# Kernel optimization log

Hardware: AMD Instinct MI355X
Metric: run time of the kernel (lower is better)

The kernel has to match this reference:

```python
import jax, jax.numpy as jnp
import numpy as np

D = 1024
T = 32768


def setup_inputs() -> dict:
    key = jax.random.key(0)
    k1, k2, k3 = jax.random.split(key, 3)
    r_star = jax.random.normal(k1, (D,), dtype=jnp.float32)
    q_t = jax.random.normal(k2, (T, D), dtype=jnp.float32)
    W = jax.random.normal(k3, (D,), dtype=jnp.float32) * (2.0 / D) ** 0.5  # ~GlorotNormal
    b = jnp.zeros((1,), dtype=jnp.float32)
    return {"r_star": r_star, "q_t": q_t, "W": W, "b": b}


def reference(r_star, q_t, W, b):
    # beta_stars[t] = W * (r_star * q_t[t]) + b  -> [T, D]
    beta = W[None, :] * (r_star[None, :] * q_t) + b  # fused elementwise
    # tf.nn.softmax default axis=-1 (over D)
    alpha = jax.nn.softmax(beta, axis=-1)  # [T, D]
    # weighted sum over the T axis -> [D]
    q_t_star = jnp.sum(alpha * q_t, axis=0)
    return q_t_star
```

## Files before the change

kernel.cpp:

```cpp
#include <hip/hip_runtime.h>
#include <math.h>

constexpr int D_   = 1024;
constexpr int T_   = 32768;
constexpr int TPB  = 512;
constexpr int WPB  = TPB / 64;
constexpr int NBLK = 512;
constexpr int TOTW = NBLK * WPB;
constexpr int ROWS = T_ / TOTW;
constexpr int NC4  = D_ / 4;

typedef float f32x4 __attribute__((ext_vector_type(4)));

__global__ __launch_bounds__(TPB) void attn_pass1_fixed(
    const float* __restrict__ r_star,
    const float* __restrict__ q_t,
    const float* __restrict__ W,
    float* __restrict__ partialT)
{
    __shared__ f32x4 lds4[WPB * NC4];

    const int tid  = threadIdx.x;
    const int lane = tid & 63;
    const int wv   = tid >> 6;
    const int gw   = blockIdx.x * WPB + wv;

    constexpr float LOG2E = 1.4426950408889634f;

    const f32x4* r4 = reinterpret_cast<const f32x4*>(r_star);
    const f32x4* w4 = reinterpret_cast<const f32x4*>(W);
    f32x4 s[4];
#pragma unroll
    for (int k = 0; k < 4; ++k)
        s[k] = r4[lane + 64 * k] * w4[lane + 64 * k] * LOG2E;

    f32x4 acc[4];
#pragma unroll
    for (int k = 0; k < 4; ++k) acc[k] = (f32x4)(0.f);

    const f32x4* qb = reinterpret_cast<const f32x4*>(q_t);
    size_t off = (size_t)gw * NC4 + lane;
    constexpr size_t STR = (size_t)TOTW * NC4;

    f32x4 q[4];
#pragma unroll
    for (int k = 0; k < 4; ++k) q[k] = qb[off + 64 * k];

#pragma unroll
    for (int i = 0; i < ROWS; ++i) {
        f32x4 qn[4];
        if (i + 1 < ROWS) {
            off += STR;
#pragma unroll
            for (int k = 0; k < 4; ++k) qn[k] = qb[off + 64 * k];
        }

        f32x4 bb[4];
#pragma unroll
        for (int k = 0; k < 4; ++k) {
            const f32x4 t = s[k] * q[k];
            bb[k].x = exp2f(t.x);
            bb[k].y = exp2f(t.y);
            bb[k].z = exp2f(t.z);
            bb[k].w = exp2f(t.w);
        }
        const float s0 = ((bb[0].x + bb[0].y) + (bb[0].z + bb[0].w))
                       + ((bb[1].x + bb[1].y) + (bb[1].z + bb[1].w));
        const float s1 = ((bb[2].x + bb[2].y) + (bb[2].z + bb[2].w))
                       + ((bb[3].x + bb[3].y) + (bb[3].z + bb[3].w));
        float ssum = s0 + s1;
#pragma unroll
        for (int o = 32; o > 0; o >>= 1)
            ssum += __shfl_xor(ssum, o, 64);

        const float inv = __builtin_amdgcn_rcpf(ssum);
#pragma unroll
        for (int k = 0; k < 4; ++k) {
            const f32x4 a = bb[k] * inv;
            acc[k].x = fmaf(a.x, q[k].x, acc[k].x);
            acc[k].y = fmaf(a.y, q[k].y, acc[k].y);
            acc[k].z = fmaf(a.z, q[k].z, acc[k].z);
            acc[k].w = fmaf(a.w, q[k].w, acc[k].w);
        }
        if (i + 1 < ROWS) {
#pragma unroll
            for (int k = 0; k < 4; ++k) q[k] = qn[k];
        }
    }

#pragma unroll
    for (int k = 0; k < 4; ++k) lds4[wv * NC4 + lane + 64 * k] = acc[k];
    __syncthreads();
    if (tid < NC4) {
        f32x4 sum = lds4[tid];
        for (int w = 1; w < WPB; ++w) sum += lds4[w * NC4 + tid];
        reinterpret_cast<f32x4*>(partialT)[(size_t)tid * NBLK + blockIdx.x] = sum;
    }
}

__global__ __launch_bounds__(TPB) void attn_pass2t(
    const float* __restrict__ partialT,
    float* __restrict__ out)
{
    __shared__ f32x4 red[TPB];
    const int tid = threadIdx.x;
    const int c   = blockIdx.x;
    red[tid] = reinterpret_cast<const f32x4*>(partialT)[(size_t)c * NBLK + tid];
    __syncthreads();
#pragma unroll
    for (int s = TPB / 2; s >= 1; s >>= 1) {
        if (tid < s) red[tid] += red[tid + s];
        __syncthreads();
    }
    if (tid == 0)
        reinterpret_cast<f32x4*>(out)[c] = red[0];
}

__global__ __launch_bounds__(TPB) void attn_pass1_generic(
    const float* __restrict__ r_star,
    const float* __restrict__ q_t,
    const float* __restrict__ W,
    float* __restrict__ partial)
{
    __shared__ f32x4 lds4[WPB * NC4];
    const int tid  = threadIdx.x;
    const int lane = tid & 63;
    const int wv   = tid >> 6;
    const int totalWaves = gridDim.x * WPB;
    const int gw = blockIdx.x * WPB + wv;
    constexpr float LOG2E = 1.4426950408889634f;

    const f32x4* r4 = reinterpret_cast<const f32x4*>(r_star);
    const f32x4* w4 = reinterpret_cast<const f32x4*>(W);
    f32x4 s[4];
#pragma unroll
    for (int k = 0; k < 4; ++k)
        s[k] = r4[lane + 64 * k] * w4[lane + 64 * k] * LOG2E;
    f32x4 acc[4];
#pragma unroll
    for (int k = 0; k < 4; ++k) acc[k] = (f32x4)(0.f);

    for (int t = gw; t < T_; t += totalWaves) {
        const f32x4* qrow = reinterpret_cast<const f32x4*>(q_t) + (size_t)t * NC4;
        f32x4 q[4];
#pragma unroll
        for (int k = 0; k < 4; ++k) q[k] = qrow[lane + 64 * k];
        f32x4 bb[4];
        float ssum = 0.f;
#pragma unroll
        for (int k = 0; k < 4; ++k) {
            const f32x4 tt = s[k] * q[k];
            bb[k].x = exp2f(tt.x); bb[k].y = exp2f(tt.y);
            bb[k].z = exp2f(tt.z); bb[k].w = exp2f(tt.w);
            ssum += (bb[k].x + bb[k].y) + (bb[k].z + bb[k].w);
        }
#pragma unroll
        for (int o = 32; o > 0; o >>= 1) ssum += __shfl_xor(ssum, o, 64);
        const float inv = __builtin_amdgcn_rcpf(ssum);
#pragma unroll
        for (int k = 0; k < 4; ++k) {
            const f32x4 a = bb[k] * inv;
            acc[k].x = fmaf(a.x, q[k].x, acc[k].x);
            acc[k].y = fmaf(a.y, q[k].y, acc[k].y);
            acc[k].z = fmaf(a.z, q[k].z, acc[k].z);
            acc[k].w = fmaf(a.w, q[k].w, acc[k].w);
        }
    }
#pragma unroll
    for (int k = 0; k < 4; ++k) lds4[wv * NC4 + lane + 64 * k] = acc[k];
    __syncthreads();
    if (tid < NC4) {
        f32x4 sum = lds4[tid];
        for (int w = 1; w < WPB; ++w) sum += lds4[w * NC4 + tid];
        reinterpret_cast<f32x4*>(partial)[(size_t)blockIdx.x * NC4 + tid] = sum;
    }
}

__global__ __launch_bounds__(256) void attn_pass2_lin(
    const float* __restrict__ partial,
    float* __restrict__ out, int nblk)
{
    __shared__ f32x4 red[256];
    const int tid = threadIdx.x;
    const int f4  = tid & 3;
    const int bg  = tid >> 2;
    const int d4b = blockIdx.x * 4;
    const f32x4* p4 = reinterpret_cast<const f32x4*>(partial);

    f32x4 acc = (f32x4)(0.f);
    for (int b = bg; b < nblk; b += 64)
        acc += p4[(size_t)b * NC4 + d4b + f4];
    red[tid] = acc;
    __syncthreads();
#pragma unroll
    for (int s = 128; s >= 4; s >>= 1) {
        if (tid < s) red[tid] += red[tid + s];
        __syncthreads();
    }
    if (tid < 4)
        reinterpret_cast<f32x4*>(out)[d4b + tid] = red[tid];
}

extern "C" void kernel_launch(void* const* d_in, const int* in_sizes, int n_in,
                              void* d_out, int out_size, void* d_ws, size_t ws_size,
                              hipStream_t stream) {
    const float* r_star = (const float*)d_in[0];
    const float* q_t    = (const float*)d_in[1];
    const float* W      = (const float*)d_in[2];
    float* out     = (float*)d_out;
    float* partial = (float*)d_ws;

    int nblk = NBLK;
    const size_t need = (size_t)NBLK * D_ * sizeof(float);
    if (ws_size >= need) {
        attn_pass1_fixed<<<NBLK, TPB, 0, stream>>>(r_star, q_t, W, partial);
        attn_pass2t<<<NC4, TPB, 0, stream>>>(partial, out);
    } else {
        nblk = (int)(ws_size / ((size_t)D_ * sizeof(float)));
        if (nblk < 1) nblk = 1;
        attn_pass1_generic<<<nblk, TPB, 0, stream>>>(r_star, q_t, W, partial);
        attn_pass2_lin<<<D_ / 16, 256, 0, stream>>>(partial, out, nblk);
    }
}
```

Measured before the change: 31.00 us.

## Use 1024-thread blocks with 256 blocks and drop manual row prefetch

The main pass now launches 256 blocks of 1024 threads instead of 512 blocks of 512, so each block holds 16 waves and the partial buffer and second reduction pass shrink by half. The explicit double-buffered prefetch of the next q row and the full loop unroll are removed, leaving latency hiding to wave-level parallelism and lowering register pressure. The generic fallback is pinned to its old 512-thread configuration. The trade-off is lost in-wave load/compute overlap and a larger LDS footprint per block, which may limit occupancy.

```diff
diff --git a/kernel.cpp b/kernel.cpp
--- a/kernel.cpp
+++ b/kernel.cpp
@@ -3,9 +3,9 @@
 
 constexpr int D_   = 1024;
 constexpr int T_   = 32768;
-constexpr int TPB  = 512;
+constexpr int TPB  = 1024;
 constexpr int WPB  = TPB / 64;
-constexpr int NBLK = 512;
+constexpr int NBLK = 256;
 constexpr int TOTW = NBLK * WPB;
 constexpr int ROWS = T_ / TOTW;
 constexpr int NC4  = D_ / 4;
@@ -42,18 +42,11 @@
     size_t off = (size_t)gw * NC4 + lane;
     constexpr size_t STR = (size_t)TOTW * NC4;
 
-    f32x4 q[4];
-#pragma unroll
-    for (int k = 0; k < 4; ++k) q[k] = qb[off + 64 * k];
-
-#pragma unroll
     for (int i = 0; i < ROWS; ++i) {
-        f32x4 qn[4];
-        if (i + 1 < ROWS) {
-            off += STR;
-#pragma unroll
-            for (int k = 0; k < 4; ++k) qn[k] = qb[off + 64 * k];
-        }
+        f32x4 q[4];
+#pragma unroll
+        for (int k = 0; k < 4; ++k) q[k] = qb[off + 64 * k];
+        off += STR;
 
         f32x4 bb[4];
 #pragma unroll
@@ -82,10 +75,6 @@
             acc[k].z = fmaf(a.z, q[k].z, acc[k].z);
             acc[k].w = fmaf(a.w, q[k].w, acc[k].w);
         }
-        if (i + 1 < ROWS) {
-#pragma unroll
-            for (int k = 0; k < 4; ++k) q[k] = qn[k];
-        }
     }
 
 #pragma unroll
@@ -93,22 +82,23 @@
     __syncthreads();
     if (tid < NC4) {
         f32x4 sum = lds4[tid];
+#pragma unroll
         for (int w = 1; w < WPB; ++w) sum += lds4[w * NC4 + tid];
         reinterpret_cast<f32x4*>(partialT)[(size_t)tid * NBLK + blockIdx.x] = sum;
     }
 }
 
-__global__ __launch_bounds__(TPB) void attn_pass2t(
+__global__ __launch_bounds__(256) void attn_pass2t(
     const float* __restrict__ partialT,
     float* __restrict__ out)
 {
-    __shared__ f32x4 red[TPB];
+    __shared__ f32x4 red[256];
     const int tid = threadIdx.x;
     const int c   = blockIdx.x;
     red[tid] = reinterpret_cast<const f32x4*>(partialT)[(size_t)c * NBLK + tid];
     __syncthreads();
 #pragma unroll
-    for (int s = TPB / 2; s >= 1; s >>= 1) {
+    for (int s = 128; s >= 1; s >>= 1) {
         if (tid < s) red[tid] += red[tid + s];
         __syncthreads();
     }
@@ -116,18 +106,18 @@
         reinterpret_cast<f32x4*>(out)[c] = red[0];
 }
 
-__global__ __launch_bounds__(TPB) void attn_pass1_generic(
+__global__ __launch_bounds__(512) void attn_pass1_generic(
     const float* __restrict__ r_star,
     const float* __restrict__ q_t,
     const float* __restrict__ W,
     float* __restrict__ partial)
 {
-    __shared__ f32x4 lds4[WPB * NC4];
+    __shared__ f32x4 lds4[8 * NC4];
     const int tid  = threadIdx.x;
     const int lane = tid & 63;
     const int wv   = tid >> 6;
-    const int totalWaves = gridDim.x * WPB;
-    const int gw = blockIdx.x * WPB + wv;
+    const int totalWaves = gridDim.x * 8;
+    const int gw = blockIdx.x * 8 + wv;
     constexpr float LOG2E = 1.4426950408889634f;
 
     const f32x4* r4 = reinterpret_cast<const f32x4*>(r_star);
@@ -171,7 +161,7 @@
     __syncthreads();
     if (tid < NC4) {
         f32x4 sum = lds4[tid];
-        for (int w = 1; w < WPB; ++w) sum += lds4[w * NC4 + tid];
+        for (int w = 1; w < 8; ++w) sum += lds4[w * NC4 + tid];
         reinterpret_cast<f32x4*>(partial)[(size_t)blockIdx.x * NC4 + tid] = sum;
     }
 }
@@ -210,15 +200,14 @@
     float* out     = (float*)d_out;
     float* partial = (float*)d_ws;
 
-    int nblk = NBLK;
     const size_t need = (size_t)NBLK * D_ * sizeof(float);
     if (ws_size >= need) {
         attn_pass1_fixed<<<NBLK, TPB, 0, stream>>>(r_star, q_t, W, partial);
-        attn_pass2t<<<NC4, TPB, 0, stream>>>(partial, out);
+        attn_pass2t<<<NC4, 256, 0, stream>>>(partial, out);
     } else {
-        nblk = (int)(ws_size / ((size_t)D_ * sizeof(float)));
+        int nblk = (int)(ws_size / ((size_t)D_ * sizeof(float)));
         if (nblk < 1) nblk = 1;
-        attn_pass1_generic<<<nblk, TPB, 0, stream>>>(r_star, q_t, W, partial);
+        attn_pass1_generic<<<nblk, 512, 0, stream>>>(r_star, q_t, W, partial);
         attn_pass2_lin<<<D_ / 16, 256, 0, stream>>>(partial, out, nblk);
     }
 }
```

After: 29.59 us, median of 2. 4.6% less time.
